# Kernel tuning notes

Hardware: AMD Instinct MI355X
Metric: run time of the kernel (lower is better)

Reference implementation:

```python
import jax, jax.numpy as jnp
import numpy as np

# ROUTER_CONFIG constants
TOP_K = 2
EXPLORATION_BONUS = 0.1
EMA_ALPHA = 0.99
B, D, E, O, CTX = 16384, 256, 8, 128, 32


def setup_inputs() -> dict:
    key = jax.random.key(0)
    ks = jax.random.split(key, 16)
    s = 0.05  # small init scale to avoid tanh saturation
    return {
        "x": jax.random.normal(ks[0], (B, D), jnp.float32),
        "targets": jax.random.normal(ks[1], (B, O), jnp.float32),
        "W1": jax.random.normal(ks[2], (D, 64), jnp.float32) * s,
        "b1": jnp.zeros((64,), jnp.float32),
        "W2": jax.random.normal(ks[3], (64, CTX), jnp.float32) * s,
        "b2": jnp.zeros((CTX,), jnp.float32),
        "S1": jax.random.normal(ks[4], (CTX, 32), jnp.float32) * s,
        "sb1": jnp.zeros((32,), jnp.float32),
        "S2": jax.random.normal(ks[5], (32, E), jnp.float32) * s,
        "sb2": jnp.zeros((E,), jnp.float32),
        "We": jax.random.normal(ks[6], (E, D, O), jnp.float32) * s,
        "be": jnp.zeros((E, O), jnp.float32),
        "expert_rewards": jax.random.normal(ks[7], (E,), jnp.float32),
        "routing_ema": jnp.ones((E,), jnp.float32) / E,
        "expert_pulls": jax.random.randint(ks[8], (E,), 0, 500, jnp.int32),
        "total_selections": 1000,
    }


def reference(x, targets, W1, b1, W2, b2, S1, sb1, S2, sb2, We, be,
              expert_rewards, routing_ema, expert_pulls, total_selections):
    # --- context encoder (dropout inactive / eval) ---
    h = jax.nn.relu(x @ W1 + b1)
    context = jnp.tanh(h @ W2 + b2)                      # [B, CTX]
    # --- expert scorer ---
    scores = jax.nn.relu(context @ S1 + sb1) @ S2 + sb2  # [B, E]
    # --- UCB terms ---
    pulls_f = expert_pulls.astype(jnp.float32)
    safe_pulls = jnp.clip(pulls_f, 1.0, None)
    explo = EXPLORATION_BONUS * jnp.sqrt(
        jnp.log(jnp.float32(total_selections)) / safe_pulls)   # [E]
    avg_reward = jnp.where(pulls_f > 0, expert_rewards / safe_pulls, 0.0)
    ucb = scores + avg_reward[None, :] + explo[None, :]   # [B, E]
    # --- top-k selection + routing weights ---
    top_vals, top_idx = jax.lax.top_k(ucb, TOP_K)         # [B, k]
    routing_w = jax.nn.softmax(top_vals, axis=1)          # [B, k]
    # --- expert forward (all experts, then gather selected) ---
    all_out = jnp.einsum('bd,edo->beo', x, We) + be       # [B, E, O]
    sel_out = jnp.take_along_axis(all_out, top_idx[:, :, None], axis=1)  # [B,k,O]
    predictions = jnp.einsum('bk,bko->bo', routing_w, sel_out)           # [B,O]
    # --- per-expert MSE losses -> rewards ---
    losses = jnp.mean((sel_out - targets[:, None, :]) ** 2, axis=-1)  # [B,k]
    rewards = -losses
    # --- vectorized bandit stat updates (replaces python loops) ---
    flat_idx = top_idx.reshape(-1)
    counts = jax.ops.segment_sum(jnp.ones_like(rewards).reshape(-1), flat_idx, num_segments=E)
    rsum = jax.ops.segment_sum(rewards.reshape(-1), flat_idx, num_segments=E)
    new_pulls = pulls_f + counts
    new_total_rewards = expert_rewards + rsum
    new_avg_reward = jnp.where(new_pulls > 0, new_total_rewards / jnp.clip(new_pulls, 1.0, None), 0.0)
    # --- routing-prob EMA update ---
    current_probs = jax.ops.segment_sum(routing_w.reshape(-1), flat_idx, num_segments=E) / x.shape[0]
    new_ema = EMA_ALPHA * routing_ema + (1.0 - EMA_ALPHA) * current_probs
    return predictions, routing_w, top_idx, new_pulls, new_avg_reward, new_ema
```

## Files before the change

### kernel.cpp

```cpp
#include <hip/hip_runtime.h>
#include <math.h>

#define B_SZ   16384
#define D_DIM  256
#define E_NUM  8
#define O_DIM  128
#define CTXW   32
#define H1     64

#define OFF_RW   2097152
#define OFF_IDX  2129920
#define OFF_NP   2162688
#define OFF_NA   2162696
#define OFF_NE   2162704

#define WS_STATS 256
#define WS_LIST  2048

__global__ __launch_bounds__(256) void zero_k(float* ws) {
    ((float4*)ws)[threadIdx.x]       = make_float4(0.f, 0.f, 0.f, 0.f);
    ((float4*)ws)[threadIdx.x + 256] = make_float4(0.f, 0.f, 0.f, 0.f);
}

__global__ __launch_bounds__(256) void score_k(
    const float* __restrict__ x,
    const float* __restrict__ W1, const float* __restrict__ b1,
    const float* __restrict__ W2, const float* __restrict__ b2,
    const float* __restrict__ S1, const float* __restrict__ sb1,
    const float* __restrict__ S2, const float* __restrict__ sb2,
    const float* __restrict__ er, const int* __restrict__ pulls,
    const int* __restrict__ tsel,
    float* __restrict__ out, int* __restrict__ wsi)
{
    __shared__ float  xs[16][D_DIM];
    __shared__ double hs[16][H1];
    __shared__ double cs[16][CTXW];
    __shared__ double tss[16][CTXW];
    __shared__ double ucb[16][E_NUM];
    __shared__ int    se[32];

    const int t = threadIdx.x, lane = t & 63, wv = t >> 6;
    const int row0 = blockIdx.x * 16;

    const float4* xsrc = (const float4*)(x + (size_t)row0 * D_DIM);
    #pragma unroll
    for (int i = 0; i < 4; ++i)
        ((float4*)xs)[t + i * 256] = xsrc[t + i * 256];
    __syncthreads();

    const int rb = wv * 4;
    {
        double a00 = (double)b1[lane], a01 = 0.0;
        double a10 = a00, a11 = 0.0;
        double a20 = a00, a21 = 0.0;
        double a30 = a00, a31 = 0.0;
        #pragma unroll 4
        for (int d = 0; d < D_DIM; d += 2) {
            float2 p0 = *(const float2*)&xs[rb + 0][d];
            float2 p1 = *(const float2*)&xs[rb + 1][d];
            float2 p2 = *(const float2*)&xs[rb + 2][d];
            float2 p3 = *(const float2*)&xs[rb + 3][d];
            double wa = (double)W1[d * H1 + lane];
            double wb = (double)W1[(d + 1) * H1 + lane];
            a00 = fma((double)p0.x, wa, a00); a01 = fma((double)p0.y, wb, a01);
            a10 = fma((double)p1.x, wa, a10); a11 = fma((double)p1.y, wb, a11);
            a20 = fma((double)p2.x, wa, a20); a21 = fma((double)p2.y, wb, a21);
            a30 = fma((double)p3.x, wa, a30); a31 = fma((double)p3.y, wb, a31);
        }
        double h0 = a00 + a01, h1 = a10 + a11, h2 = a20 + a21, h3 = a30 + a31;
        hs[rb + 0][lane] = h0 > 0.0 ? h0 : 0.0;
        hs[rb + 1][lane] = h1 > 0.0 ? h1 : 0.0;
        hs[rb + 2][lane] = h2 > 0.0 ? h2 : 0.0;
        hs[rb + 3][lane] = h3 > 0.0 ? h3 : 0.0;
    }
    __syncthreads();

    {
        const int unit = lane & 31, half = lane >> 5;
        const int ra = rb + half * 2;
        double c0 = (double)b2[unit], c1 = c0;
        #pragma unroll 4
        for (int k = 0; k < H1; ++k) {
            double w2v = (double)W2[k * CTXW + unit];
            c0 = fma(hs[ra][k], w2v, c0);
            c1 = fma(hs[ra + 1][k], w2v, c1);
        }
        cs[ra][unit] = tanh(c0);
        cs[ra + 1][unit] = tanh(c1);
    }
    __syncthreads();

    {
        const int unit = lane & 31, half = lane >> 5;
        const int ra = rb + half * 2;
        double a0 = (double)sb1[unit], a1 = a0;
        #pragma unroll 4
        for (int k = 0; k < CTXW; ++k) {
            double s1v = (double)S1[k * CTXW + unit];
            a0 = fma(cs[ra][k], s1v, a0);
            a1 = fma(cs[ra + 1][k], s1v, a1);
        }
        tss[ra][unit]     = a0 > 0.0 ? a0 : 0.0;
        tss[ra + 1][unit] = a1 > 0.0 ? a1 : 0.0;
    }
    __syncthreads();

    if (lane < 32) {
        const int e = lane & 7, r = rb + (lane >> 3);
        double a = (double)sb2[e];
        #pragma unroll 4
        for (int k = 0; k < CTXW; ++k)
            a = fma(tss[r][k], (double)S2[k * E_NUM + e], a);
        double pf = (double)pulls[e];
        double sp = pf < 1.0 ? 1.0 : pf;
        double explo = 0.1 * sqrt(log((double)(*tsel)) / sp);
        double avg = pf > 0.0 ? (double)er[e] / sp : 0.0;
        ucb[r][e] = a + avg + explo;
    }
    __syncthreads();

    if (t < 16) {
        double u[E_NUM];
        #pragma unroll
        for (int e = 0; e < E_NUM; ++e) u[e] = ucb[t][e];
        int i0 = 0; double v0 = u[0];
        #pragma unroll
        for (int e = 1; e < E_NUM; ++e) if (u[e] > v0) { v0 = u[e]; i0 = e; }
        int i1 = -1; double v1 = -1.0e300;
        #pragma unroll
        for (int e = 0; e < E_NUM; ++e) {
            if (e == i0) continue;
            if (u[e] > v1) { v1 = u[e]; i1 = e; }
        }
        double exd = exp(v1 - v0);
        double w0 = 1.0 / (1.0 + exd), w1 = exd / (1.0 + exd);
        int row = row0 + t;
        out[OFF_RW  + row * 2]     = (float)w0;
        out[OFF_RW  + row * 2 + 1] = (float)w1;
        out[OFF_IDX + row * 2]     = (float)i0;
        out[OFF_IDX + row * 2 + 1] = (float)i1;
        se[t * 2]     = i0;
        se[t * 2 + 1] = i1;
    }
    __syncthreads();

    if (t < 16) {
        const int e = t & 7, slot = t >> 3;
        int cntl = 0;
        for (int j = slot; j < 32; j += 2) cntl += (se[j] == e);
        if (cntl) {
            int base = atomicAdd(&wsi[slot * 8 + e], cntl);
            int k = 0;
            if (slot == 0) {
                for (int j = 0; j < 32; j += 2)
                    if (se[j] == e)
                        wsi[WS_LIST + e * B_SZ + base + (k++)] = row0 + (j >> 1);
            } else {
                for (int j = 1; j < 32; j += 2)
                    if (se[j] == e)
                        wsi[WS_LIST + e * B_SZ + (B_SZ - 1 - base - (k++))] = row0 + (j >> 1);
            }
        }
    }
}

template <int SLOT>
__global__ __launch_bounds__(256) void expert_k(
    const float* __restrict__ x, const float* __restrict__ tgt,
    const float* __restrict__ We, const float* __restrict__ be,
    float* out, int* __restrict__ wsi, float* __restrict__ wsf)
{
    const int e = blockIdx.x >> 9, chunk = blockIdx.x & 511;
    const int cnt = wsi[SLOT * 8 + e];
    const int base = chunk * 32;
    if (base >= cnt) return;

    __shared__ float xsl[32][68];
    __shared__ float wes[64][O_DIM];
    __shared__ int   rowid[32];
    __shared__ float wsl[32];
    __shared__ float be_sh[O_DIM];

    const int t = threadIdx.x;
    if (t < 32) {
        bool ok = (base + t) < cnt;
        int row = -1;
        if (ok) {
            int idx = (SLOT == 0) ? (base + t) : (B_SZ - 1 - (base + t));
            row = wsi[WS_LIST + e * B_SZ + idx];
        }
        rowid[t] = row;
        wsl[t]   = ok ? out[OFF_RW + row * 2 + SLOT] : 0.f;
    }
    if (t < O_DIM) be_sh[t] = be[e * O_DIM + t];

    float acc[4][4];
    #pragma unroll
    for (int r = 0; r < 4; ++r)
        #pragma unroll
        for (int j = 0; j < 4; ++j) acc[r][j] = 0.f;

    const int tx = t & 31, ty = t >> 5;
    const int o4 = tx * 4;

    for (int k0 = 0; k0 < 4; ++k0) {
        __syncthreads();
        const float4* wsrc = (const float4*)(We + ((size_t)e * D_DIM + k0 * 64) * O_DIM);
        #pragma unroll
        for (int i = 0; i < 8; ++i)
            ((float4*)wes)[t + i * 256] = wsrc[t + i * 256];
        {
            int r = t >> 3, seg = t & 7;
            int rr = rowid[r] < 0 ? 0 : rowid[r];
            const float* xsr = x + (size_t)rr * D_DIM + k0 * 64 + seg * 8;
            *(float4*)&xsl[r][seg * 8]     = *(const float4*)(xsr);
            *(float4*)&xsl[r][seg * 8 + 4] = *(const float4*)(xsr + 4);
        }
        __syncthreads();
        #pragma unroll 4
        for (int kq = 0; kq < 16; ++kq) {
            float4 w0 = *(float4*)&wes[kq * 4 + 0][o4];
            float4 w1 = *(float4*)&wes[kq * 4 + 1][o4];
            float4 w2 = *(float4*)&wes[kq * 4 + 2][o4];
            float4 w3 = *(float4*)&wes[kq * 4 + 3][o4];
            #pragma unroll
            for (int r = 0; r < 4; ++r) {
                float4 xv = *(float4*)&xsl[ty * 4 + r][kq * 4];
                acc[r][0] = fmaf(xv.x, w0.x, acc[r][0]);
                acc[r][1] = fmaf(xv.x, w0.y, acc[r][1]);
                acc[r][2] = fmaf(xv.x, w0.z, acc[r][2]);
                acc[r][3] = fmaf(xv.x, w0.w, acc[r][3]);
                acc[r][0] = fmaf(xv.y, w1.x, acc[r][0]);
                acc[r][1] = fmaf(xv.y, w1.y, acc[r][1]);
                acc[r][2] = fmaf(xv.y, w1.z, acc[r][2]);
                acc[r][3] = fmaf(xv.y, w1.w, acc[r][3]);
                acc[r][0] = fmaf(xv.z, w2.x, acc[r][0]);
                acc[r][1] = fmaf(xv.z, w2.y, acc[r][1]);
                acc[r][2] = fmaf(xv.z, w2.z, acc[r][2]);
                acc[r][3] = fmaf(xv.z, w2.w, acc[r][3]);
                acc[r][0] = fmaf(xv.w, w3.x, acc[r][0]);
                acc[r][1] = fmaf(xv.w, w3.y, acc[r][1]);
                acc[r][2] = fmaf(xv.w, w3.z, acc[r][2]);
                acc[r][3] = fmaf(xv.w, w3.w, acc[r][3]);
            }
        }
    }

    float cntl = 0.f, rsl = 0.f, wsuml = 0.f;
    #pragma unroll
    for (int r = 0; r < 4; ++r) {
        int li = ty * 4 + r;
        int row = rowid[li];
        bool valid = row >= 0;
        float w = wsl[li];
        float4 tg = make_float4(0.f, 0.f, 0.f, 0.f);
        if (valid) tg = *(const float4*)(tgt + (size_t)row * O_DIM + o4);
        float cf0 = acc[r][0] + be_sh[o4 + 0];
        float cf1 = acc[r][1] + be_sh[o4 + 1];
        float cf2 = acc[r][2] + be_sh[o4 + 2];
        float cf3 = acc[r][3] + be_sh[o4 + 3];
        float d0 = cf0 - tg.x, d1 = cf1 - tg.y, d2 = cf2 - tg.z, d3 = cf3 - tg.w;
        float lpr = d0 * d0 + d1 * d1 + d2 * d2 + d3 * d3;
        if (valid) {
            float* pr = out + (size_t)row * O_DIM + o4;
            if (SLOT == 0) {
                float4 v = make_float4(w * cf0, w * cf1, w * cf2, w * cf3);
                *(float4*)pr = v;
            } else {
                float4 p = *(const float4*)pr;
                p.x += w * cf0; p.y += w * cf1; p.z += w * cf2; p.w += w * cf3;
                *(float4*)pr = p;
            }
        }
        #pragma unroll
        for (int off = 1; off < 32; off <<= 1)
            lpr += __shfl_xor(lpr, off, 64);
        if (tx == 0 && valid) {
            cntl += 1.f;
            rsl  += -(lpr * (1.0f / 128.0f));
            wsuml += w;
        }
    }
    if (tx == 0) {
        int cp = WS_STATS + (blockIdx.x & 63) * 24;
        if (cntl > 0.f) {
            atomicAdd(&wsf[cp + e], cntl);
            atomicAdd(&wsf[cp + 8 + e], rsl);
            atomicAdd(&wsf[cp + 16 + e], wsuml);
        }
    }
}

__global__ void final_k(const float* __restrict__ er,
                        const float* __restrict__ ema,
                        const int* __restrict__ pulls,
                        const float* __restrict__ wsf,
                        float* __restrict__ out)
{
    int e = threadIdx.x;
    if (e < E_NUM) {
        double c = 0.0, rs = 0.0, wsum = 0.0;
        for (int cp = 0; cp < 64; ++cp) {
            c    += (double)wsf[WS_STATS + cp * 24 + e];
            rs   += (double)wsf[WS_STATS + cp * 24 + 8 + e];
            wsum += (double)wsf[WS_STATS + cp * 24 + 16 + e];
        }
        double pf = (double)pulls[e];
        double npl = pf + c;
        double ntr = (double)er[e] + rs;
        double sp = npl < 1.0 ? 1.0 : npl;
        double navg = npl > 0.0 ? ntr / sp : 0.0;
        double prob = wsum / (double)B_SZ;
        double nema = 0.99 * (double)ema[e] + 0.01 * prob;
        out[OFF_NP + e] = (float)npl;
        out[OFF_NA + e] = (float)navg;
        out[OFF_NE + e] = (float)nema;
    }
}

extern "C" void kernel_launch(void* const* d_in, const int* in_sizes, int n_in,
                              void* d_out, int out_size, void* d_ws, size_t ws_size,
                              hipStream_t stream) {
    const float* x    = (const float*)d_in[0];
    const float* tgt  = (const float*)d_in[1];
    const float* W1   = (const float*)d_in[2];
    const float* b1   = (const float*)d_in[3];
    const float* W2   = (const float*)d_in[4];
    const float* b2   = (const float*)d_in[5];
    const float* S1   = (const float*)d_in[6];
    const float* sb1  = (const float*)d_in[7];
    const float* S2   = (const float*)d_in[8];
    const float* sb2  = (const float*)d_in[9];
    const float* We   = (const float*)d_in[10];
    const float* be   = (const float*)d_in[11];
    const float* erw  = (const float*)d_in[12];
    const float* ema  = (const float*)d_in[13];
    const int*   pulls = (const int*)d_in[14];
    const int*   tsel  = (const int*)d_in[15];
    float* out = (float*)d_out;
    float* wsf = (float*)d_ws;
    int*   wsi = (int*)d_ws;

    zero_k<<<1, 256, 0, stream>>>(wsf);
    score_k<<<B_SZ / 16, 256, 0, stream>>>(
        x, W1, b1, W2, b2, S1, sb1, S2, sb2, erw, pulls, tsel, out, wsi);
    expert_k<0><<<E_NUM * 512, 256, 0, stream>>>(x, tgt, We, be, out, wsi, wsf);
    expert_k<1><<<E_NUM * 512, 256, 0, stream>>>(x, tgt, We, be, out, wsi, wsf);
    final_k<<<1, 64, 0, stream>>>(erw, ema, pulls, wsf, out);
}
```

Before: 199.1 us.

## Fuse both top-k slot expert passes into one launch with temp buffer and combine

Runs the slot-0 and slot-1 expert GEMM passes in a single grid of twice the size. Slot 1 writes its weighted output to a workspace temp buffer instead of doing a read-modify-write on the output, and a separate combine kernel then sums the two. This removes the serialization between the two expert launches and raises parallelism, at the cost of an extra 8MB write and read plus one more launch. It also replaces the zeroing kernel with hipMemsetAsync. The fused path is used only when the workspace is large enough, otherwise the old two-launch path runs.

Result: no change. 196.5 us (-1.3%).

```diff
diff --git a/kernel.cpp b/kernel.cpp
--- a/kernel.cpp
+++ b/kernel.cpp
@@ -16,11 +16,8 @@
 
 #define WS_STATS 256
 #define WS_LIST  2048
-
-__global__ __launch_bounds__(256) void zero_k(float* ws) {
-    ((float4*)ws)[threadIdx.x]       = make_float4(0.f, 0.f, 0.f, 0.f);
-    ((float4*)ws)[threadIdx.x + 256] = make_float4(0.f, 0.f, 0.f, 0.f);
-}
+#define WS_TMP   1048576
+#define WS_NEED  ((size_t)(WS_TMP + B_SZ * O_DIM) * 4)
 
 __global__ __launch_bounds__(256) void score_k(
     const float* __restrict__ x,
@@ -164,14 +161,16 @@
     }
 }
 
-template <int SLOT>
+template <int FUSED, int SLOTP>
 __global__ __launch_bounds__(256) void expert_k(
     const float* __restrict__ x, const float* __restrict__ tgt,
     const float* __restrict__ We, const float* __restrict__ be,
-    float* out, int* __restrict__ wsi, float* __restrict__ wsf)
+    float* out, int* __restrict__ wsi, float* __restrict__ wsf,
+    float* __restrict__ tmp)
 {
-    const int e = blockIdx.x >> 9, chunk = blockIdx.x & 511;
-    const int cnt = wsi[SLOT * 8 + e];
+    const int slot = FUSED ? (blockIdx.x >> 12) : SLOTP;
+    const int e = (blockIdx.x >> 9) & 7, chunk = blockIdx.x & 511;
+    const int cnt = wsi[slot * 8 + e];
     const int base = chunk * 32;
     if (base >= cnt) return;
 
@@ -186,11 +185,11 @@
         bool ok = (base + t) < cnt;
         int row = -1;
         if (ok) {
-            int idx = (SLOT == 0) ? (base + t) : (B_SZ - 1 - (base + t));
+            int idx = (slot == 0) ? (base + t) : (B_SZ - 1 - (base + t));
             row = wsi[WS_LIST + e * B_SZ + idx];
         }
         rowid[t] = row;
-        wsl[t]   = ok ? out[OFF_RW + row * 2 + SLOT] : 0.f;
+        wsl[t]   = ok ? out[OFF_RW + row * 2 + slot] : 0.f;
     }
     if (t < O_DIM) be_sh[t] = be[e * O_DIM + t];
 
@@ -262,14 +261,18 @@
         float d0 = cf0 - tg.x, d1 = cf1 - tg.y, d2 = cf2 - tg.z, d3 = cf3 - tg.w;
         float lpr = d0 * d0 + d1 * d1 + d2 * d2 + d3 * d3;
         if (valid) {
-            float* pr = out + (size_t)row * O_DIM + o4;
-            if (SLOT == 0) {
-                float4 v = make_float4(w * cf0, w * cf1, w * cf2, w * cf3);
-                *(float4*)pr = v;
+            if (FUSED) {
+                float* pr = (slot == 0 ? out : tmp) + (size_t)row * O_DIM + o4;
+                *(float4*)pr = make_float4(w * cf0, w * cf1, w * cf2, w * cf3);
             } else {
-                float4 p = *(const float4*)pr;
-                p.x += w * cf0; p.y += w * cf1; p.z += w * cf2; p.w += w * cf3;
-                *(float4*)pr = p;
+                float* pr = out + (size_t)row * O_DIM + o4;
+                if (SLOTP == 0) {
+                    *(float4*)pr = make_float4(w * cf0, w * cf1, w * cf2, w * cf3);
+                } else {
+                    float4 p = *(const float4*)pr;
+                    p.x += w * cf0; p.y += w * cf1; p.z += w * cf2; p.w += w * cf3;
+                    *(float4*)pr = p;
+                }
             }
         }
         #pragma unroll
@@ -289,6 +292,14 @@
             atomicAdd(&wsf[cp + 16 + e], wsuml);
         }
     }
+}
+
+__global__ __launch_bounds__(256) void combine_k(float* out, const float* __restrict__ tmp) {
+    int i = blockIdx.x * 256 + threadIdx.x;
+    float4 p = ((const float4*)out)[i];
+    float4 q = ((const float4*)tmp)[i];
+    p.x += q.x; p.y += q.y; p.z += q.z; p.w += q.w;
+    ((float4*)out)[i] = p;
 }
 
 __global__ void final_k(const float* __restrict__ er,
@@ -340,11 +351,20 @@
     float* out = (float*)d_out;
     float* wsf = (float*)d_ws;
     int*   wsi = (int*)d_ws;
-
-    zero_k<<<1, 256, 0, stream>>>(wsf);
+    float* tmp = wsf + WS_TMP;
+
+    hipMemsetAsync(d_ws, 0, 8192, stream);
     score_k<<<B_SZ / 16, 256, 0, stream>>>(
         x, W1, b1, W2, b2, S1, sb1, S2, sb2, erw, pulls, tsel, out, wsi);
-    expert_k<0><<<E_NUM * 512, 256, 0, stream>>>(x, tgt, We, be, out, wsi, wsf);
-    expert_k<1><<<E_NUM * 512, 256, 0, stream>>>(x, tgt, We, be, out, wsi, wsf);
+    if (ws_size >= WS_NEED) {
+        expert_k<1, 0><<<2 * E_NUM * 512, 256, 0, stream>>>(
+            x, tgt, We, be, out, wsi, wsf, tmp);
+        combine_k<<<2048, 256, 0, stream>>>(out, tmp);
+    } else {
+        expert_k<0, 0><<<E_NUM * 512, 256, 0, stream>>>(
+            x, tgt, We, be, out, wsi, wsf, tmp);
+        expert_k<0, 1><<<E_NUM * 512, 256, 0, stream>>>(
+            x, tgt, We, be, out, wsi, wsf, tmp);
+    }
     final_k<<<1, 64, 0, stream>>>(erw, ema, pulls, wsf, out);
 }
```
